# Kernel tuning notes

Hardware: AMD Instinct MI355X
Metric: run time of the kernel (lower is better)

The kernel has to match this reference:

```python
import jax, jax.numpy as jnp
import numpy as np

T, B, D, H, O = 512, 64, 1024, 1024, 1024
N_LAYERS = 2


def setup_inputs() -> dict:
    key = jax.random.key(0)
    ks = jax.random.split(key, 1 + 4 * N_LAYERS)
    inp = {
        "x": jax.random.normal(ks[0], (T, B, D), dtype=jnp.float32),
        "paddings": jnp.zeros((T, B, 1), dtype=jnp.float32),
    }
    d_in = D
    for i in range(N_LAYERS):
        s_ih = 1.0 / np.sqrt(d_in)
        s_hh = 1.0 / np.sqrt(H)
        inp[f"Wih{i}"] = jax.random.normal(ks[1 + 4 * i], (d_in, 3 * H), jnp.float32) * s_ih
        inp[f"Whh{i}"] = jax.random.normal(ks[2 + 4 * i], (H, 3 * H), jnp.float32) * s_hh
        inp[f"b{i}"] = jnp.zeros((3 * H,), jnp.float32)
        inp[f"Who{i}"] = jax.random.normal(ks[3 + 4 * i], (H, O), jnp.float32) * s_hh
        d_in = O
    return inp


def _gru_layer(x, p, Wih, Whh, b, Who):
    # x: [T, B, D_in], p: [T, B, 1]
    Bsz = x.shape[1]
    Hd = Whh.shape[0]
    # precompute input-side gates for all steps: [T, B, 3H]
    gx_all = jnp.einsum("tbd,dk->tbk", x, Wih) + b

    def step(h, inp):
        gx, pt = inp  # gx: [B, 3H], pt: [B, 1]
        gh = h @ Whh  # [B, 3H]
        r = jax.nn.sigmoid(gx[:, :Hd] + gh[:, :Hd])
        z = jax.nn.sigmoid(gx[:, Hd:2 * Hd] + gh[:, Hd:2 * Hd])
        n = jnp.tanh(gx[:, 2 * Hd:] + r * gh[:, 2 * Hd:])
        h_new = (1.0 - z) * n + z * h
        h_new = pt * h + (1.0 - pt) * h_new  # padded steps keep state
        return h_new, h_new

    h0 = jnp.zeros((Bsz, Hd), x.dtype)
    _, hs = jax.lax.scan(step, h0, (gx_all, p))  # hs: [T, B, H]
    return jnp.einsum("tbh,ho->tbo", hs, Who)


def reference(x, paddings, Wih0, Whh0, b0, Who0, Wih1, Whh1, b1, Who1):
    layers = [(Wih0, Whh0, b0, Who0), (Wih1, Whh1, b1, Who1)]
    xs = x
    for (Wih, Whh, b, Who) in layers:
        xs = _gru_layer(xs, paddings, Wih, Whh, b, Who)
    return xs
```

## Files before the change

### kernel.cpp

```cpp
#include <hip/hip_runtime.h>
#include <hip/hip_bf16.h>

typedef __bf16 bf16;
typedef __bf16 bf16x8 __attribute__((ext_vector_type(8)));
typedef float  f32x4  __attribute__((ext_vector_type(4)));
typedef unsigned long long u64;
typedef unsigned short u16;

__global__ __launch_bounds__(256) void cast_f32_bf16(const float* __restrict__ in,
                                                     bf16* __restrict__ out) {
    size_t i = ((size_t)blockIdx.x * blockDim.x + threadIdx.x) * 8;
    float4 a = *(const float4*)(in + i);
    float4 b = *(const float4*)(in + i + 4);
    bf16x8 o;
    o[0] = (bf16)a.x; o[1] = (bf16)a.y; o[2] = (bf16)a.z; o[3] = (bf16)a.w;
    o[4] = (bf16)b.x; o[5] = (bf16)b.y; o[6] = (bf16)b.z; o[7] = (bf16)b.w;
    *(bf16x8*)(out + i) = o;
}

__global__ __launch_bounds__(256) void transpose_cast(const float* __restrict__ in,
                                                      bf16* __restrict__ out,
                                                      int R, int C) {
    __shared__ float tile[32][33];
    int c0 = blockIdx.x * 32, r0 = blockIdx.y * 32;
    int tx = threadIdx.x & 31, ty = threadIdx.x >> 5;
    #pragma unroll
    for (int i = 0; i < 32; i += 8)
        tile[ty + i][tx] = in[(size_t)(r0 + ty + i) * C + c0 + tx];
    __syncthreads();
    #pragma unroll
    for (int i = 0; i < 32; i += 8)
        out[(size_t)(c0 + ty + i) * R + r0 + tx] = (bf16)tile[tx][ty + i];
}

template<bool BF16_OUT, bool HAS_BIAS>
__global__ __launch_bounds__(256) void gemm128(const bf16* __restrict__ A,
                                               const bf16* __restrict__ Bt,
                                               const float* __restrict__ bias,
                                               void* __restrict__ Cout,
                                               int M, int N, int K) {
    __shared__ bf16 sA[128][72];
    __shared__ bf16 sB[128][72];
    const int tid = threadIdx.x, lane = tid & 63, w = tid >> 6;
    const int wr = w >> 1, wc = w & 1;
    const int m0 = blockIdx.y * 128, n0 = blockIdx.x * 128;
    const int ml = lane & 15, kb = (lane >> 4) * 8;

    f32x4 acc[4][4] = {};
    const bf16* Ab = A  + (size_t)m0 * K;
    const bf16* Bb = Bt + (size_t)n0 * K;

    for (int kc = 0; kc < K; kc += 64) {
        #pragma unroll
        for (int i = 0; i < 4; ++i) {
            int c = tid + 256 * i;
            int row = c >> 3, col = (c & 7) * 8;
            *(uint4*)&sA[row][col] = *(const uint4*)(Ab + (size_t)row * K + kc + col);
            *(uint4*)&sB[row][col] = *(const uint4*)(Bb + (size_t)row * K + kc + col);
        }
        __syncthreads();
        #pragma unroll
        for (int ks = 0; ks < 2; ++ks) {
            bf16x8 af[4], bfr[4];
            #pragma unroll
            for (int i = 0; i < 4; ++i)
                af[i] = *(const bf16x8*)&sA[wr * 64 + i * 16 + ml][ks * 32 + kb];
            #pragma unroll
            for (int i = 0; i < 4; ++i)
                bfr[i] = *(const bf16x8*)&sB[wc * 64 + i * 16 + ml][ks * 32 + kb];
            #pragma unroll
            for (int mi = 0; mi < 4; ++mi)
                #pragma unroll
                for (int ni = 0; ni < 4; ++ni)
                    acc[mi][ni] = __builtin_amdgcn_mfma_f32_16x16x32_bf16(
                        af[mi], bfr[ni], acc[mi][ni], 0, 0, 0);
        }
        __syncthreads();
    }
    const int rbase = (lane >> 4) * 4;
    #pragma unroll
    for (int mi = 0; mi < 4; ++mi) {
        #pragma unroll
        for (int ni = 0; ni < 4; ++ni) {
            int col = n0 + wc * 64 + ni * 16 + ml;
            float bv = HAS_BIAS ? bias[col] : 0.f;
            #pragma unroll
            for (int r = 0; r < 4; ++r) {
                int row = m0 + wr * 64 + mi * 16 + rbase + r;
                float v = acc[mi][ni][r] + bv;
                if constexpr (BF16_OUT)
                    ((bf16*)Cout)[(size_t)row * N + col] = (bf16)v;
                else
                    ((float*)Cout)[(size_t)row * N + col] = v;
            }
        }
    }
}

__device__ __forceinline__ void mm_step(const char* sW, const bf16* hsrc,
                                        int myrow, int kb, int ml, f32x4 acc[3]) {
    const char* rowp = (const char*)(hsrc + (size_t)myrow * 1024) + kb * 2;
    uint4 hq[32];
    #pragma unroll
    for (int ks = 0; ks < 32; ++ks)
        asm volatile("global_load_dwordx4 %0, %1, off"
                     : "=v"(hq[ks]) : "v"(rowp + ks * 64) : "memory");
    asm volatile("s_waitcnt vmcnt(16)" ::: "memory");
    __builtin_amdgcn_sched_barrier(0);
    #pragma unroll
    for (int ks = 0; ks < 16; ++ks) {
        bf16x8 af = __builtin_bit_cast(bf16x8, hq[ks]);
        #pragma unroll
        for (int g = 0; g < 3; ++g) {
            int brow = g * 16 + ml;
            int addr = brow * 2048 + (ks * 32 + kb) * 2;
            addr ^= (brow & 7) << 4;
            bf16x8 bw = *(const bf16x8*)(sW + addr);
            acc[g] = __builtin_amdgcn_mfma_f32_16x16x32_bf16(af, bw, acc[g], 0, 0, 0);
        }
    }
    asm volatile("s_waitcnt vmcnt(0)" ::: "memory");
    __builtin_amdgcn_sched_barrier(0);
    #pragma unroll
    for (int ks = 16; ks < 32; ++ks) {
        bf16x8 af = __builtin_bit_cast(bf16x8, hq[ks]);
        #pragma unroll
        for (int g = 0; g < 3; ++g) {
            int brow = g * 16 + ml;
            int addr = brow * 2048 + (ks * 32 + kb) * 2;
            addr ^= (brow & 7) << 4;
            bf16x8 bw = *(const bf16x8*)(sW + addr);
            acc[g] = __builtin_amdgcn_mfma_f32_16x16x32_bf16(af, bw, acc[g], 0, 0, 0);
        }
    }
}

__device__ __forceinline__ void store_pair_sc(bf16* base, size_t idx,
                                              unsigned short v, int ml) {
    unsigned nb = (unsigned)__shfl_xor((int)(unsigned)v, 1, 64);
    if ((ml & 1) == 0) {
        unsigned pk = (unsigned)v | (nb << 16);
        __hip_atomic_store((unsigned*)(base + idx), pk,
                           __ATOMIC_RELAXED, __HIP_MEMORY_SCOPE_AGENT);
    }
}

__device__ __forceinline__ void poll1(const u16* a, unsigned ta, int lane) {
    while (true) {
        unsigned fa = (unsigned)__hip_atomic_load(a + lane, __ATOMIC_RELAXED,
                                                  __HIP_MEMORY_SCOPE_AGENT);
        if (__all((int)(fa >= ta))) break;
        __builtin_amdgcn_s_sleep(8);
    }
    asm volatile("" ::: "memory");
}

__device__ __forceinline__ void publish1(u16* s1, unsigned val, int lane) {
    asm volatile("s_waitcnt vmcnt(0)" ::: "memory");
    if (lane == 0)
        __hip_atomic_store(s1, (u16)val, __ATOMIC_RELAXED, __HIP_MEMORY_SCOPE_AGENT);
}
__device__ __forceinline__ void publish2(u16* s1, u16* s2, unsigned val, int lane) {
    asm volatile("s_waitcnt vmcnt(0)" ::: "memory");
    if (lane == 0) {
        __hip_atomic_store(s1, (u16)val, __ATOMIC_RELAXED, __HIP_MEMORY_SCOPE_AGENT);
        __hip_atomic_store(s2, (u16)val, __ATOMIC_RELAXED, __HIP_MEMORY_SCOPE_AGENT);
    }
}

__global__ __launch_bounds__(256, 1) void gru_fused(
    const bf16* __restrict__ WH1T, const bf16* __restrict__ W2fT,
    const bf16* __restrict__ WH2T, const bf16* __restrict__ gx1,
    const float* __restrict__ pad, const float* __restrict__ b2,
    bf16* __restrict__ h1,
    bf16* __restrict__ gx2ring,
    bf16* __restrict__ hs2,
    u16* __restrict__ f1s, u16* __restrict__ f1c,
    u16* __restrict__ f2,
    u16* __restrict__ f3s, u16* __restrict__ f3c) {
    extern __shared__ __align__(16) char sW[];

    const int tid = threadIdx.x, lane = tid & 63, wv = tid >> 6;
    const int role = blockIdx.x >> 6, jg = blockIdx.x & 63;
    const int j0 = jg * 16;
    const int ml = lane & 15, kb = (lane >> 4) * 8;
    const int rbase = (lane >> 4) * 4;
    const int myrow = wv * 16 + ml;
    const int bbase = wv * 16 + rbase;
    const int jml = j0 + ml;

    const bf16* Wsrc = (role == 0) ? WH1T : (role == 1) ? W2fT : WH2T;
    #pragma unroll 1
    for (int i = 0; i < 24; ++i) {
        int c = tid + 256 * i;
        int rr = c >> 7;
        int off = (c & 127) * 16;
        int gate = rr >> 4, j = rr & 15;
        const bf16* src = Wsrc + (size_t)(gate * 1024 + j0 + j) * 1024 + off / 2;
        *(uint4*)(sW + rr * 2048 + (off ^ ((rr & 7) << 4))) = *(const uint4*)src;
    }
    __syncthreads();

    if (role == 0) {
        u16* fown = f1s + wv * 64;
        float hreg[4] = {0.f, 0.f, 0.f, 0.f};
        float gxv[12]; float4 pv;
        #pragma unroll
        for (int r = 0; r < 4; ++r) {
            size_t b = (size_t)(bbase + r);
            gxv[r * 3 + 0] = (float)gx1[b * 3072 + jml];
            gxv[r * 3 + 1] = (float)gx1[b * 3072 + 1024 + jml];
            gxv[r * 3 + 2] = (float)gx1[b * 3072 + 2048 + jml];
        }
        pv = *(const float4*)(pad + bbase);

        for (int t = 0; t < 512; ++t) {
            f32x4 acc[3] = {};
            if (t > 0) {
                poll1(fown, (unsigned)t, lane);
                mm_step(sW, h1 + (size_t)(t - 1) * 65536, myrow, kb, ml, acc);
            }
            unsigned short hpk[4];
            #pragma unroll
            for (int r = 0; r < 4; ++r) {
                float rr = 1.f / (1.f + __expf(-(gxv[r * 3 + 0] + acc[0][r])));
                float zz = 1.f / (1.f + __expf(-(gxv[r * 3 + 1] + acc[1][r])));
                float nn = tanhf(gxv[r * 3 + 2] + rr * acc[2][r]);
                float hold = hreg[r];
                float hn = (1.f - zz) * nn + zz * hold;
                float p = (r == 0) ? pv.x : (r == 1) ? pv.y : (r == 2) ? pv.z : pv.w;
                hn = p * hold + (1.f - p) * hn;
                hreg[r] = hn;
                hpk[r] = __builtin_bit_cast(unsigned short, (bf16)hn);
            }
            bf16* hst = h1 + (size_t)t * 65536;
            #pragma unroll
            for (int r = 0; r < 4; ++r)
                store_pair_sc(hst, (size_t)(bbase + r) * 1024 + jml, hpk[r], ml);
            publish2(fown + jg, f1c + wv * 64 + jg, (unsigned)(t + 1), lane);
            {
                int tn = (t < 511) ? t + 1 : 511;
                const bf16* gxt = gx1 + (size_t)tn * 64 * 3072;
                #pragma unroll
                for (int r = 0; r < 4; ++r) {
                    size_t b = (size_t)(bbase + r);
                    gxv[r * 3 + 0] = (float)gxt[b * 3072 + jml];
                    gxv[r * 3 + 1] = (float)gxt[b * 3072 + 1024 + jml];
                    gxv[r * 3 + 2] = (float)gxt[b * 3072 + 2048 + jml];
                }
                pv = *(const float4*)(pad + tn * 64 + bbase);
            }
        }
    } else if (role == 1) {
        u16* fsrc = f1c + wv * 64;
        u16* fbp  = f3c + wv * 64;
        for (int t = 0; t < 512; ++t) {
            poll1(fsrc, (unsigned)(t + 1), lane);
            f32x4 acc[3] = {};
            mm_step(sW, h1 + (size_t)t * 65536, myrow, kb, ml, acc);
            if (t >= 16)
                poll1(fbp, (unsigned)(t - 15), lane);
            bf16* dst = gx2ring + (size_t)(t & 15) * 196608;
            #pragma unroll
            for (int g = 0; g < 3; ++g) {
                unsigned short w0 = __builtin_bit_cast(unsigned short, (bf16)acc[g][0]);
                unsigned short w1 = __builtin_bit_cast(unsigned short, (bf16)acc[g][1]);
                unsigned short w2 = __builtin_bit_cast(unsigned short, (bf16)acc[g][2]);
                unsigned short w3 = __builtin_bit_cast(unsigned short, (bf16)acc[g][3]);
                u64 pk = (u64)w0 | ((u64)w1 << 16) | ((u64)w2 << 32) | ((u64)w3 << 48);
                __hip_atomic_store((u64*)(dst + ((size_t)(g * 1024 + jml)) * 64 + bbase),
                                   pk, __ATOMIC_RELAXED, __HIP_MEMORY_SCOPE_AGENT);
            }
            publish1(f2 + wv * 64 + jg, (unsigned)(t + 1), lane);
        }
    } else {
        u16* fown = f3s + wv * 64;
        u16* fgx  = f2 + wv * 64;
        float b2v[3] = {b2[jml], b2[1024 + jml], b2[2048 + jml]};
        float hreg[4] = {0.f, 0.f, 0.f, 0.f};
        float4 pv = *(const float4*)(pad + bbase);

        for (int t = 0; t < 512; ++t) {
            poll1(fgx, (unsigned)(t + 1), lane);
            const bf16* gsl = gx2ring + (size_t)(t & 15) * 196608;
            u64 gq[3];
            #pragma unroll
            for (int g = 0; g < 3; ++g)
                gq[g] = __hip_atomic_load(
                    (const u64*)(gsl + ((size_t)(g * 1024 + jml)) * 64 + bbase),
                    __ATOMIC_RELAXED, __HIP_MEMORY_SCOPE_AGENT);
            f32x4 acc[3] = {};
            if (t > 0) {
                poll1(fown, (unsigned)t, lane);
                mm_step(sW, hs2 + (size_t)(t - 1) * 65536, myrow, kb, ml, acc);
            }
            unsigned short hpk[4];
            #pragma unroll
            for (int r = 0; r < 4; ++r) {
                float gr = (float)__builtin_bit_cast(bf16,
                    (unsigned short)(gq[0] >> (r * 16))) + b2v[0];
                float gz = (float)__builtin_bit_cast(bf16,
                    (unsigned short)(gq[1] >> (r * 16))) + b2v[1];
                float gn = (float)__builtin_bit_cast(bf16,
                    (unsigned short)(gq[2] >> (r * 16))) + b2v[2];
                float rr = 1.f / (1.f + __expf(-(gr + acc[0][r])));
                float zz = 1.f / (1.f + __expf(-(gz + acc[1][r])));
                float nn = tanhf(gn + rr * acc[2][r]);
                float hold = hreg[r];
                float hn = (1.f - zz) * nn + zz * hold;
                float p = (r == 0) ? pv.x : (r == 1) ? pv.y : (r == 2) ? pv.z : pv.w;
                hn = p * hold + (1.f - p) * hn;
                hreg[r] = hn;
                hpk[r] = __builtin_bit_cast(unsigned short, (bf16)hn);
            }
            bf16* hst = hs2 + (size_t)t * 65536;
            #pragma unroll
            for (int r = 0; r < 4; ++r)
                store_pair_sc(hst, (size_t)(bbase + r) * 1024 + jml, hpk[r], ml);
            publish2(fown + jg, f3c + wv * 64 + jg, (unsigned)(t + 1), lane);
            int tn = (t < 511) ? t + 1 : 511;
            pv = *(const float4*)(pad + tn * 64 + bbase);
        }
    }
}

extern "C" void kernel_launch(void* const* d_in, const int* in_sizes, int n_in,
                              void* d_out, int out_size, void* d_ws, size_t ws_size,
                              hipStream_t stream) {
    const float* x    = (const float*)d_in[0];
    const float* pad  = (const float*)d_in[1];
    const float* Wih1 = (const float*)d_in[2];
    const float* Whh1 = (const float*)d_in[3];
    const float* b1   = (const float*)d_in[4];
    const float* Who1 = (const float*)d_in[5];
    const float* Wih2 = (const float*)d_in[6];
    const float* Whh2 = (const float*)d_in[7];
    const float* b2   = (const float*)d_in[8];
    const float* Who2 = (const float*)d_in[9];
    float* out_f = (float*)d_out;

    char* p = (char*)d_ws;
    bf16* xb      = (bf16*)p; p += (size_t)32768 * 1024 * 2;
    bf16* gxb     = (bf16*)p; p += (size_t)32768 * 3072 * 2;
    bf16* h1      = (bf16*)p; p += (size_t)32768 * 1024 * 2;
    bf16* hs2     = (bf16*)p; p += (size_t)32768 * 1024 * 2;
    bf16* gx2ring = (bf16*)p; p += (size_t)16 * 196608 * 2;
    bf16* WT1     = (bf16*)p; p += (size_t)3072 * 1024 * 2;
    bf16* who1b   = (bf16*)p; p += (size_t)1024 * 1024 * 2;
    bf16* W2fT    = (bf16*)p; p += (size_t)3072 * 1024 * 2;
    bf16* WH1     = (bf16*)p; p += (size_t)3072 * 1024 * 2;
    bf16* WH2     = (bf16*)p; p += (size_t)3072 * 1024 * 2;
    u16* flags = (u16*)p; p += 8192;
    u16* f1s = flags,        * f1c = flags + 256;
    u16* f2  = flags + 512;
    u16* f3s = flags + 768,  * f3c = flags + 1024;

    hipFuncSetAttribute((const void*)gru_fused,
                        hipFuncAttributeMaxDynamicSharedMemorySize, 131072);

    cast_f32_bf16<<<16384, 256, 0, stream>>>(x, xb);
    transpose_cast<<<dim3(96, 32), 256, 0, stream>>>(Wih1, WT1, 1024, 3072);
    gemm128<true, true><<<dim3(24, 256), 256, 0, stream>>>(
        xb, WT1, b1, gxb, 32768, 3072, 1024);
    transpose_cast<<<dim3(96, 32), 256, 0, stream>>>(Wih2, WT1, 1024, 3072);
    cast_f32_bf16<<<512, 256, 0, stream>>>(Who1, who1b);
    gemm128<true, false><<<dim3(8, 24), 256, 0, stream>>>(
        WT1, who1b, nullptr, W2fT, 3072, 1024, 1024);
    transpose_cast<<<dim3(96, 32), 256, 0, stream>>>(Whh1, WH1, 1024, 3072);
    transpose_cast<<<dim3(96, 32), 256, 0, stream>>>(Whh2, WH2, 1024, 3072);
    transpose_cast<<<dim3(32, 32), 256, 0, stream>>>(Who2, WT1, 1024, 1024);
    hipMemsetAsync(flags, 0, 8192, stream);
    gru_fused<<<192, 256, 98304, stream>>>(WH1, W2fT, WH2, gxb, pad, b2,
                                           h1, gx2ring, hs2,
                                           f1s, f1c, f2, f3s, f3c);
    gemm128<false, false><<<dim3(8, 256), 256, 0, stream>>>(
        hs2, WT1, nullptr, out_f, 32768, 1024, 1024);
}
```

Baseline: 5.285 ms.

## Store recurrent hidden states in MFMA-fragment layout for coalesced per-step loads

Hidden states exchanged between blocks each step are now written in a layout that matches the MFMA A-fragment order. Each lane's 32 per-step loads then hit contiguous 1KB spans instead of strided row-major rows. Layer 2 uses a 16-slot fragment ring for its recurrence and also writes a separate row-major copy for the final output GEMM. This adds an extra store per step in layer 2 in exchange for cheaper loads on the serial critical path.

After: 4.763 ms (median of 2 runs). 9.9% less time.

```diff
diff --git a/kernel.cpp b/kernel.cpp
--- a/kernel.cpp
+++ b/kernel.cpp
@@ -97,14 +97,15 @@
     }
 }
 
-__device__ __forceinline__ void mm_step(const char* sW, const bf16* hsrc,
-                                        int myrow, int kb, int ml, f32x4 acc[3]) {
-    const char* rowp = (const char*)(hsrc + (size_t)myrow * 1024) + kb * 2;
+__device__ __forceinline__ void mm_step(const char* sW, const char* hslot,
+                                        int wv, int lane, int kb, int ml,
+                                        f32x4 acc[3]) {
+    const char* rowp = hslot + wv * 32768 + (lane >> 4) * 256 + ml * 16;
     uint4 hq[32];
     #pragma unroll
     for (int ks = 0; ks < 32; ++ks)
         asm volatile("global_load_dwordx4 %0, %1, off"
-                     : "=v"(hq[ks]) : "v"(rowp + ks * 64) : "memory");
+                     : "=v"(hq[ks]) : "v"(rowp + ks * 1024) : "memory");
     asm volatile("s_waitcnt vmcnt(16)" ::: "memory");
     __builtin_amdgcn_sched_barrier(0);
     #pragma unroll
@@ -135,12 +136,14 @@
     }
 }
 
-__device__ __forceinline__ void store_pair_sc(bf16* base, size_t idx,
-                                              unsigned short v, int ml) {
+__device__ __forceinline__ void store_pair_frag(char* slot, int b, int j,
+                                                unsigned short v, int ml) {
     unsigned nb = (unsigned)__shfl_xor((int)(unsigned)v, 1, 64);
     if ((ml & 1) == 0) {
         unsigned pk = (unsigned)v | (nb << 16);
-        __hip_atomic_store((unsigned*)(base + idx), pk,
+        size_t off = (size_t)((b >> 4) * 32768 + (j >> 5) * 1024 +
+                              ((j >> 3) & 3) * 256 + (b & 15) * 16 + (j & 7) * 2);
+        __hip_atomic_store((unsigned*)(slot + off), pk,
                            __ATOMIC_RELAXED, __HIP_MEMORY_SCOPE_AGENT);
     }
 }
@@ -172,9 +175,10 @@
     const bf16* __restrict__ WH1T, const bf16* __restrict__ W2fT,
     const bf16* __restrict__ WH2T, const bf16* __restrict__ gx1,
     const float* __restrict__ pad, const float* __restrict__ b2,
-    bf16* __restrict__ h1,
+    char* __restrict__ h1f,
     bf16* __restrict__ gx2ring,
-    bf16* __restrict__ hs2,
+    char* __restrict__ hs2f,
+    bf16* __restrict__ hs2row,
     u16* __restrict__ f1s, u16* __restrict__ f1c,
     u16* __restrict__ f2,
     u16* __restrict__ f3s, u16* __restrict__ f3c) {
@@ -185,7 +189,6 @@
     const int j0 = jg * 16;
     const int ml = lane & 15, kb = (lane >> 4) * 8;
     const int rbase = (lane >> 4) * 4;
-    const int myrow = wv * 16 + ml;
     const int bbase = wv * 16 + rbase;
     const int jml = j0 + ml;
 
@@ -218,7 +221,7 @@
             f32x4 acc[3] = {};
             if (t > 0) {
                 poll1(fown, (unsigned)t, lane);
-                mm_step(sW, h1 + (size_t)(t - 1) * 65536, myrow, kb, ml, acc);
+                mm_step(sW, h1f + (size_t)(t - 1) * 131072, wv, lane, kb, ml, acc);
             }
             unsigned short hpk[4];
             #pragma unroll
@@ -233,10 +236,10 @@
                 hreg[r] = hn;
                 hpk[r] = __builtin_bit_cast(unsigned short, (bf16)hn);
             }
-            bf16* hst = h1 + (size_t)t * 65536;
+            char* hst = h1f + (size_t)t * 131072;
             #pragma unroll
             for (int r = 0; r < 4; ++r)
-                store_pair_sc(hst, (size_t)(bbase + r) * 1024 + jml, hpk[r], ml);
+                store_pair_frag(hst, bbase + r, jml, hpk[r], ml);
             publish2(fown + jg, f1c + wv * 64 + jg, (unsigned)(t + 1), lane);
             {
                 int tn = (t < 511) ? t + 1 : 511;
@@ -257,7 +260,7 @@
         for (int t = 0; t < 512; ++t) {
             poll1(fsrc, (unsigned)(t + 1), lane);
             f32x4 acc[3] = {};
-            mm_step(sW, h1 + (size_t)t * 65536, myrow, kb, ml, acc);
+            mm_step(sW, h1f + (size_t)t * 131072, wv, lane, kb, ml, acc);
             if (t >= 16)
                 poll1(fbp, (unsigned)(t - 15), lane);
             bf16* dst = gx2ring + (size_t)(t & 15) * 196608;
@@ -292,7 +295,7 @@
             f32x4 acc[3] = {};
             if (t > 0) {
                 poll1(fown, (unsigned)t, lane);
-                mm_step(sW, hs2 + (size_t)(t - 1) * 65536, myrow, kb, ml, acc);
+                mm_step(sW, hs2f + (size_t)((t - 1) & 15) * 131072, wv, lane, kb, ml, acc);
             }
             unsigned short hpk[4];
             #pragma unroll
@@ -313,10 +316,19 @@
                 hreg[r] = hn;
                 hpk[r] = __builtin_bit_cast(unsigned short, (bf16)hn);
             }
-            bf16* hst = hs2 + (size_t)t * 65536;
+            char* hstf = hs2f + (size_t)(t & 15) * 131072;
             #pragma unroll
             for (int r = 0; r < 4; ++r)
-                store_pair_sc(hst, (size_t)(bbase + r) * 1024 + jml, hpk[r], ml);
+                store_pair_frag(hstf, bbase + r, jml, hpk[r], ml);
+            bf16* hstr = hs2row + (size_t)t * 65536;
+            #pragma unroll
+            for (int r = 0; r < 4; ++r) {
+                unsigned nb = (unsigned)__shfl_xor((int)(unsigned)hpk[r], 1, 64);
+                if ((ml & 1) == 0) {
+                    unsigned pk = (unsigned)hpk[r] | (nb << 16);
+                    *(unsigned*)(hstr + (size_t)(bbase + r) * 1024 + jml) = pk;
+                }
+            }
             publish2(fown + jg, f3c + wv * 64 + jg, (unsigned)(t + 1), lane);
             int tn = (t < 511) ? t + 1 : 511;
             pv = *(const float4*)(pad + tn * 64 + bbase);
@@ -342,8 +354,9 @@
     char* p = (char*)d_ws;
     bf16* xb      = (bf16*)p; p += (size_t)32768 * 1024 * 2;
     bf16* gxb     = (bf16*)p; p += (size_t)32768 * 3072 * 2;
-    bf16* h1      = (bf16*)p; p += (size_t)32768 * 1024 * 2;
-    bf16* hs2     = (bf16*)p; p += (size_t)32768 * 1024 * 2;
+    char* h1f     = p;        p += (size_t)512 * 131072;
+    bf16* hs2row  = (bf16*)p; p += (size_t)32768 * 1024 * 2;
+    char* hs2f    = p;        p += (size_t)16 * 131072;
     bf16* gx2ring = (bf16*)p; p += (size_t)16 * 196608 * 2;
     bf16* WT1     = (bf16*)p; p += (size_t)3072 * 1024 * 2;
     bf16* who1b   = (bf16*)p; p += (size_t)1024 * 1024 * 2;
@@ -371,8 +384,8 @@
     transpose_cast<<<dim3(32, 32), 256, 0, stream>>>(Who2, WT1, 1024, 1024);
     hipMemsetAsync(flags, 0, 8192, stream);
     gru_fused<<<192, 256, 98304, stream>>>(WH1, W2fT, WH2, gxb, pad, b2,
-                                           h1, gx2ring, hs2,
+                                           h1f, gx2ring, hs2f, hs2row,
                                            f1s, f1c, f2, f3s, f3c);
     gemm128<false, false><<<dim3(8, 256), 256, 0, stream>>>(
-        hs2, WT1, nullptr, out_f, 32768, 1024, 1024);
-}
+        hs2row, WT1, nullptr, out_f, 32768, 1024, 1024);
+}
```
